# Kernel optimization log

Hardware: AMD Instinct MI355X
Metric: run time of the kernel (lower is better)

## Reference

```python
import jax, jax.numpy as jnp
import numpy as np

EMB = 1024
HEADS = 16


def setup_inputs() -> dict:
    key = jax.random.key(0)
    k1, k2, k3, k4, k5 = jax.random.split(key, 5)
    b, n = 2, 2048
    x = jax.random.normal(k1, (b, n, EMB), dtype=jnp.float32)
    Wqkv = jax.random.normal(k2, (EMB, 3 * EMB), dtype=jnp.float32) * (EMB ** -0.5)
    bqkv = jax.random.normal(k3, (3 * EMB,), dtype=jnp.float32) * 0.02
    Wproj = jax.random.normal(k4, (EMB, EMB), dtype=jnp.float32) * (EMB ** -0.5)
    bproj = jax.random.normal(k5, (EMB,), dtype=jnp.float32) * 0.02
    return {"x": x, "Wqkv": Wqkv, "bqkv": bqkv, "Wproj": Wproj, "bproj": bproj}


def reference(x, Wqkv, bqkv, Wproj, bproj):
    b, n, e = x.shape
    h = HEADS
    d = e // h
    qkv = x @ Wqkv + bqkv                      # [b, n, 3e]
    # rearrange 'b n (h d qkv) -> qkv b h n d' : qkv index is innermost
    qkv = qkv.reshape(b, n, h, d, 3)
    qkv = jnp.transpose(qkv, (4, 0, 2, 1, 3))  # [3, b, h, n, d]
    q, k, v = qkv[0], qkv[1], qkv[2]
    energy = jnp.einsum('bhqd,bhkd->bhqk', q, k)
    scaling = jnp.float32(e) ** 0.5            # NOTE: sqrt(emb_size), not head_dim
    att = jax.nn.softmax(energy / scaling, axis=-1)
    out = jnp.einsum('bhql,bhld->bhqd', att, v)
    out = jnp.transpose(out, (0, 2, 1, 3)).reshape(b, n, e)  # 'b h n d -> b n (h d)'
    return out @ Wproj + bproj
```

## Files before the change

kernel.cpp:

```cpp
#include <hip/hip_runtime.h>
#include <hip/hip_bf16.h>
#include <stdint.h>

typedef __bf16 bf16;
typedef __attribute__((ext_vector_type(8))) __bf16 bf16x8;
typedef __attribute__((ext_vector_type(4))) __bf16 bf16x4;
typedef __attribute__((ext_vector_type(4))) float f32x4;
typedef __attribute__((ext_vector_type(16))) float f32x16;

#define MFMA16(a, b, c) __builtin_amdgcn_mfma_f32_16x16x32_bf16((a), (b), (c), 0, 0, 0)
#define MFMA32(a, b, c) __builtin_amdgcn_mfma_f32_32x32x16_bf16((a), (b), (c), 0, 0, 0)

#define QSCALE 0.045084220027780106f

__device__ __forceinline__ void glds16(const void* g, void* l) {
  __builtin_amdgcn_global_load_lds(
      (const __attribute__((address_space(1))) void*)g,
      (__attribute__((address_space(3))) void*)l, 16, 0, 0);
}

__device__ __forceinline__ bf16x8 ldsfrag(const unsigned char* base, int row, int colb) {
  return *(const bf16x8*)(base + row * 128 + (colb ^ ((row & 7) << 4)));
}

__device__ __forceinline__ uint32_t pkbf16(float a, float b) {
  uint32_t r;
  asm("v_cvt_pk_bf16_f32 %0, %1, %2" : "=v"(r) : "v"(a), "v"(b));
  return r;
}

__device__ __forceinline__ float fexp2(float x) {
#if __has_builtin(__builtin_amdgcn_exp2f)
  return __builtin_amdgcn_exp2f(x);
#else
  float r;
  asm("v_exp_f32 %0, %1" : "=v"(r) : "v"(x));
  return r;
#endif
}

__device__ __forceinline__ f32x16 zero16() {
  f32x16 v;
#pragma unroll
  for (int i = 0; i < 16; ++i) v[i] = 0.f;
  return v;
}

__global__ __launch_bounds__(256) void k_prep_x(const float* __restrict__ x, bf16* __restrict__ xb) {
  int gid = blockIdx.x * 256 + threadIdx.x;
  const f32x4* xv = (const f32x4*)x;
  f32x4 a = xv[(size_t)gid * 2], b = xv[(size_t)gid * 2 + 1];
  bf16x8 o;
#pragma unroll
  for (int i = 0; i < 4; ++i) { o[i] = (bf16)a[i]; o[i + 4] = (bf16)b[i]; }
  *(bf16x8*)(xb + (size_t)gid * 8) = o;
}

template <int MODE>
__global__ __launch_bounds__(256) void k_prep_w(const float* __restrict__ W, bf16* __restrict__ WT) {
  __shared__ float tile[64][256];
  const int C = (MODE == 0) ? 3072 : 1024;
  const int c0 = blockIdx.x * 256, k0 = blockIdx.y * 64;
  const int lw = threadIdx.x & 63, w = threadIdx.x >> 6;
#pragma unroll
  for (int i = 0; i < 16; ++i) {
    int r = i * 4 + w;
    f32x4 v = *(const f32x4*)(W + (size_t)(k0 + r) * C + c0 + lw * 4);
    *(f32x4*)&tile[r][lw * 4] = v;
  }
  __syncthreads();
  const int c = c0 + threadIdx.x;
  int j;
  float sc = 1.0f;
  if (MODE == 0) {
    int h = c / 192, rem = c - h * 192, dd = rem / 3, wh = rem - dd * 3;
    j = wh * 1024 + h * 64 + dd;
    if (wh == 0) sc = QSCALE;
  } else {
    j = c;
  }
#pragma unroll
  for (int ch = 0; ch < 8; ++ch) {
    bf16x8 o;
#pragma unroll
    for (int i = 0; i < 8; ++i) o[i] = (bf16)(tile[ch * 8 + i][threadIdx.x] * sc);
    *(bf16x8*)(WT + (size_t)j * 1024 + k0 + ch * 8) = o;
  }
}

__global__ __launch_bounds__(256) void k_prep_bias(const float* __restrict__ bqkv, float* __restrict__ bp) {
  int gid = blockIdx.x * 256 + threadIdx.x;
  int wj = gid >> 10, rr = gid & 1023, hh = rr >> 6, d2 = rr & 63;
  float v = bqkv[hh * 192 + d2 * 3 + wj];
  bp[gid] = (wj == 0) ? v * QSCALE : v;
}

template <int EPI>
__global__ __launch_bounds__(256) void k_gemm(const bf16* __restrict__ A, const bf16* __restrict__ BT,
                                              const float* __restrict__ bias, bf16* __restrict__ qk,
                                              bf16* __restrict__ vt, float* __restrict__ outf) {
  __shared__ __align__(16) unsigned char sA[16384];
  __shared__ __align__(16) unsigned char sB[16384];
  const int tid = threadIdx.x;
  const int l = tid & 63, w = tid >> 6, g = l >> 4, l15 = l & 15;
  const int wr = w >> 1, wc = w & 1;
  const int bm = blockIdx.y, bn = blockIdx.x;
  const unsigned char* Ab = (const unsigned char*)A + (size_t)bm * 128 * 2048;
  const unsigned char* Bb = (const unsigned char*)BT + (size_t)bn * 128 * 2048;
  f32x4 acc[4][4];
#pragma unroll
  for (int mi = 0; mi < 4; ++mi)
#pragma unroll
    for (int ni = 0; ni < 4; ++ni) acc[mi][ni] = (f32x4){0.f, 0.f, 0.f, 0.f};

  for (int kt = 0; kt < 16; ++kt) {
    const int k0b = kt * 128;
#pragma unroll
    for (int p = 0; p < 4; ++p) {
      int co = (p * 256 + tid) * 16;
      int row = co >> 7, wb = co & 127;
      int sw = wb ^ ((row & 7) << 4);
      glds16(Ab + (size_t)row * 2048 + k0b + sw, sA + co);
      glds16(Bb + (size_t)row * 2048 + k0b + sw, sB + co);
    }
    __syncthreads();
#pragma unroll
    for (int ks = 0; ks < 2; ++ks) {
      bf16x8 af[4], bfr[4];
#pragma unroll
      for (int mi = 0; mi < 4; ++mi) af[mi] = ldsfrag(sA, wr * 64 + mi * 16 + l15, ks * 64 + g * 16);
#pragma unroll
      for (int ni = 0; ni < 4; ++ni) bfr[ni] = ldsfrag(sB, wc * 64 + ni * 16 + l15, ks * 64 + g * 16);
      __builtin_amdgcn_s_setprio(1);
#pragma unroll
      for (int mi = 0; mi < 4; ++mi)
#pragma unroll
        for (int ni = 0; ni < 4; ++ni) acc[mi][ni] = MFMA16(af[mi], bfr[ni], acc[mi][ni]);
      __builtin_amdgcn_s_setprio(0);
    }
    __syncthreads();
  }
#pragma unroll
  for (int ni = 0; ni < 4; ++ni) {
    int j = bn * 128 + wc * 64 + ni * 16 + l15;
    float bj = bias[j];
#pragma unroll
    for (int mi = 0; mi < 4; ++mi) {
      int m0 = bm * 128 + wr * 64 + mi * 16 + g * 4;
      float v[4];
#pragma unroll
      for (int rr = 0; rr < 4; ++rr) v[rr] = acc[mi][ni][rr] + bj;
      if (EPI == 0) {
        int which = j >> 10, r = j & 1023, h = r >> 6, dd = r & 63;
        int b = m0 >> 11, nn = m0 & 2047;
        if (which < 2) {
#pragma unroll
          for (int rr = 0; rr < 4; ++rr)
            qk[(size_t)which * 4194304 + (((size_t)b * 16 + h) * 2048 + nn + rr) * 64 + dd] = (bf16)v[rr];
        } else {
          bf16x4 pw = {(bf16)v[0], (bf16)v[1], (bf16)v[2], (bf16)v[3]};
          *(bf16x4*)(vt + (((size_t)b * 16 + h) * 64 + dd) * 2048 + nn) = pw;
        }
      } else {
#pragma unroll
        for (int rr = 0; rr < 4; ++rr) outf[(size_t)(m0 + rr) * 1024 + j] = v[rr];
      }
    }
  }
}

__global__ __launch_bounds__(256, 2) void k_attn(const bf16* __restrict__ Qg, const bf16* __restrict__ Kg,
                                                 const bf16* __restrict__ VTg, bf16* __restrict__ Og) {
  __shared__ __align__(16) unsigned char smem[66560];
  const int tid = threadIdx.x;
  const int l = tid & 63, w = tid >> 6;
  const int q = l & 31, hi = l >> 5;
  const int g = w >> 1, wl = w & 1;
  const int stid = tid & 127;

  const int bid = blockIdx.x;
  const int wg = (bid & 7) * 64 + (bid >> 3);
  const int bh = wg >> 4;
  const int q0w = (wg & 15) * 128 + wl * 64;

  bf16x8 qf[2][4];
#pragma unroll
  for (int qt = 0; qt < 2; ++qt)
#pragma unroll
    for (int ks = 0; ks < 4; ++ks)
      qf[qt][ks] = *(const bf16x8*)(Qg + ((size_t)bh * 2048 + q0w + qt * 32 + q) * 64 + ks * 16 + hi * 8);

  f32x16 oacc[2][2];
#pragma unroll
  for (int qt = 0; qt < 2; ++qt) { oacc[qt][0] = zero16(); oacc[qt][1] = zero16(); }
  float lrun4[2][4] = {{0.f, 0.f, 0.f, 0.f}, {0.f, 0.f, 0.f, 0.f}};
  bf16x8 pb[2][4];

  const unsigned char* Kb = (const unsigned char*)Kg + (size_t)bh * 262144 + (size_t)g * 131072;
  const unsigned char* Vb = (const unsigned char*)VTg + (size_t)bh * 262144 + (size_t)g * 2048;
  unsigned char* sKg = smem + g * 16384;
  unsigned char* sVg = smem + 32768 + g * 16384;

  int sco[4], ssw[4];
  size_t svoff[4];
#pragma unroll
  for (int i = 0; i < 4; ++i) {
    sco[i] = stid * 16 + i * 2048;
    int row = sco[i] >> 7;
    ssw[i] = (sco[i] & 127) ^ ((row & 7) << 4);
    svoff[i] = (size_t)row * 4096 + ssw[i];
  }

#define STAGE_K(kb_, buf_)                                                        \
  do {                                                                            \
    const unsigned char* Ksrc = Kb + (size_t)(kb_) * 8192;                        \
    _Pragma("unroll") for (int i = 0; i < 4; ++i)                                 \
      glds16(Ksrc + (sco[i] & ~127) + ssw[i], sKg + (buf_) * 8192 + sco[i]);      \
  } while (0)
#define STAGE_V(kb_, buf_)                                                        \
  do {                                                                            \
    _Pragma("unroll") for (int i = 0; i < 4; ++i)                                 \
      glds16(Vb + svoff[i] + (size_t)(kb_) * 128, sVg + (buf_) * 8192 + sco[i]);  \
  } while (0)

#define QK_EXP_PACK(kbase_)                                                       \
  do {                                                                            \
    _Pragma("unroll") for (int kt = 0; kt < 2; ++kt) {                            \
      bf16x8 kf[4];                                                               \
      _Pragma("unroll") for (int ks = 0; ks < 4; ++ks)                            \
        kf[ks] = ldsfrag((kbase_), kt * 32 + q, ks * 32 + hi * 16);               \
      _Pragma("unroll") for (int qt = 0; qt < 2; ++qt) {                          \
        f32x16 sacc = zero16();                                                   \
        __builtin_amdgcn_s_setprio(1);                                            \
        _Pragma("unroll") for (int ks = 0; ks < 4; ++ks)                          \
          sacc = MFMA32(kf[ks], qf[qt][ks], sacc);                                \
        __builtin_amdgcn_s_setprio(0);                                            \
        float pe[16];                                                             \
        _Pragma("unroll") for (int r = 0; r < 16; ++r) pe[r] = fexp2(sacc[r]);    \
        _Pragma("unroll") for (int m = 0; m < 4; ++m)                             \
          _Pragma("unroll") for (int j = 0; j < 4; ++j) lrun4[qt][j] += pe[4 * m + j]; \
        uint32_t c[4][2];                                                         \
        _Pragma("unroll") for (int m = 0; m < 4; ++m) {                           \
          c[m][0] = pkbf16(pe[4 * m], pe[4 * m + 1]);                             \
          c[m][1] = pkbf16(pe[4 * m + 2], pe[4 * m + 3]);                         \
        }                                                                         \
        _Pragma("unroll") for (int s = 0; s < 2; ++s) {                           \
          uint32_t x0 = c[2 * s][0], y0 = c[2 * s + 1][0];                        \
          uint32_t x1 = c[2 * s][1], y1 = c[2 * s + 1][1];                        \
          asm("v_permlane32_swap_b32 %0, %1" : "+v"(x0), "+v"(y0));               \
          asm("v_permlane32_swap_b32 %0, %1" : "+v"(x1), "+v"(y1));               \
          union { uint32_t u[4]; bf16x8 v; } bfr;                                 \
          bfr.u[0] = x0; bfr.u[1] = x1; bfr.u[2] = y0; bfr.u[3] = y1;             \
          pb[qt][kt * 2 + s] = bfr.v;                                             \
        }                                                                         \
      }                                                                           \
    }                                                                             \
  } while (0)

#define PV_TILE(vbase_)                                                           \
  do {                                                                            \
    __builtin_amdgcn_s_setprio(1);                                                \
    _Pragma("unroll") for (int ks = 0; ks < 4; ++ks)                              \
      _Pragma("unroll") for (int dt = 0; dt < 2; ++dt) {                          \
        bf16x8 vf = ldsfrag((vbase_), dt * 32 + q, ks * 32 + hi * 16);            \
        _Pragma("unroll") for (int qt = 0; qt < 2; ++qt)                          \
          oacc[qt][dt] = MFMA32(vf, pb[qt][ks], oacc[qt][dt]);                    \
      }                                                                           \
    __builtin_amdgcn_s_setprio(0);                                                \
  } while (0)

  STAGE_K(0, 0);
  STAGE_V(0, 0);
  __syncthreads();
  STAGE_K(1, 1);
  QK_EXP_PACK(sKg);
  __syncthreads();
  int cur = 0;

  for (int kb = 0; kb < 15; ++kb) {
    const int nxt = cur ^ 1;
    if (kb < 14) STAGE_K(kb + 2, cur);
    STAGE_V(kb + 1, nxt);
    PV_TILE(sVg + cur * 8192);
    QK_EXP_PACK(sKg + nxt * 8192);
    __syncthreads();
    cur = nxt;
  }
  PV_TILE(sVg + cur * 8192);

#undef STAGE_K
#undef STAGE_V
#undef QK_EXP_PACK
#undef PV_TILE

  float lrun[2];
#pragma unroll
  for (int qt = 0; qt < 2; ++qt)
    lrun[qt] = (lrun4[qt][0] + lrun4[qt][1]) + (lrun4[qt][2] + lrun4[qt][3]);

  float* mbuf = (float*)smem;
  float* lb = (float*)(smem + 65536);
  if (g == 1) {
#pragma unroll
    for (int qt = 0; qt < 2; ++qt) {
#pragma unroll
      for (int dt = 0; dt < 2; ++dt)
#pragma unroll
        for (int r = 0; r < 16; ++r)
          mbuf[((wl * 64 + qt * 32 + dt * 16 + r) << 6) + l] = oacc[qt][dt][r];
      lb[(wl * 2 + qt) * 64 + l] = lrun[qt];
    }
  }
  __syncthreads();
  if (g == 0) {
#pragma unroll
    for (int qt = 0; qt < 2; ++qt)
#pragma unroll
      for (int dt = 0; dt < 2; ++dt)
#pragma unroll
        for (int r = 0; r < 16; ++r)
          oacc[qt][dt][r] += mbuf[((wl * 64 + qt * 32 + dt * 16 + r) << 6) + l];
  }
  __syncthreads();
  if (g == 0) {
    const int b = bh >> 4, h = bh & 15;
    unsigned char* sO = smem + 32768 + wl * 4096;
#pragma unroll
    for (int qt = 0; qt < 2; ++qt) {
      float lr = lrun[qt] + lb[(wl * 2 + qt) * 64 + l];
      float ps = lr + __shfl_xor(lr, 32);
      float linv = 1.0f / ps;
#pragma unroll
      for (int dt = 0; dt < 2; ++dt)
#pragma unroll
        for (int m = 0; m < 4; ++m) {
          uint32_t b0 = pkbf16(oacc[qt][dt][4 * m] * linv, oacc[qt][dt][4 * m + 1] * linv);
          uint32_t b1 = pkbf16(oacc[qt][dt][4 * m + 2] * linv, oacc[qt][dt][4 * m + 3] * linv);
          int byteo = (dt * 64 + m * 16 + hi * 8) ^ ((q & 7) << 4);
          uint32_t* dst = (uint32_t*)(sO + q * 128 + byteo);
          dst[0] = b0; dst[1] = b1;
        }
      const int q0 = q0w + qt * 32;
#pragma unroll
      for (int rd = 0; rd < 4; ++rd) {
        int byteo = hi * 64 + rd * 16;
        bf16x8 v = *(const bf16x8*)(sO + q * 128 + (byteo ^ ((q & 7) << 4)));
        *(bf16x8*)(Og + ((size_t)b * 2048 + q0 + q) * 1024 + h * 64 + byteo / 2) = v;
      }
    }
  }
}

extern "C" void kernel_launch(void* const* d_in, const int* in_sizes, int n_in,
                              void* d_out, int out_size, void* d_ws, size_t ws_size,
                              hipStream_t stream) {
  const float* x = (const float*)d_in[0];
  const float* Wqkv = (const float*)d_in[1];
  const float* bqkv = (const float*)d_in[2];
  const float* Wproj = (const float*)d_in[3];
  const float* bproj = (const float*)d_in[4];
  float* out = (float*)d_out;
  char* ws = (char*)d_ws;

  bf16* XB = (bf16*)(ws + 0);
  bf16* WQT = (bf16*)(ws + 8388608);
  float* BQP = (float*)(ws + 14680064);
  bf16* WPT = (bf16*)(ws + 14696448);
  bf16* Q = (bf16*)(ws + 16793600);
  bf16* K = (bf16*)(ws + 25182208);
  bf16* VT = (bf16*)(ws + 33570816);
  bf16* AO = XB;
  (void)K;
  (void)ws_size;

  k_prep_x<<<2048, 256, 0, stream>>>(x, XB);
  k_prep_w<0><<<dim3(12, 16), 256, 0, stream>>>(Wqkv, WQT);
  k_prep_w<1><<<dim3(4, 16), 256, 0, stream>>>(Wproj, WPT);
  k_prep_bias<<<12, 256, 0, stream>>>(bqkv, BQP);
  k_gemm<0><<<dim3(24, 32), 256, 0, stream>>>(XB, WQT, BQP, Q, VT, nullptr);
  k_attn<<<512, 256, 0, stream>>>(Q, Q + 4194304, VT, AO);
  k_gemm<1><<<dim3(8, 32), 256, 0, stream>>>(AO, WPT, bproj, nullptr, nullptr, out);
}
```

Baseline: 125.3 us.

## Interleave PV MFMAs with QK/exp work using ping-pong probability registers

The main attention loop now interleaves the PV matrix multiplies for the previous key block with the QK scores and exponentials of the next block inside one fused iteration. Probabilities go into two alternating register sets (pbA/pbB), and the loop is unrolled by two so the buffer indices are compile-time constants. The aim is to hide exp/pack VALU latency behind MFMA work and give the scheduler more overlap. In exchange it needs more VGPRs for the second probability buffer, which could lower occupancy or cause spills.

```diff
diff --git a/kernel.cpp b/kernel.cpp
--- a/kernel.cpp
+++ b/kernel.cpp
@@ -194,7 +194,7 @@
 #pragma unroll
   for (int qt = 0; qt < 2; ++qt) { oacc[qt][0] = zero16(); oacc[qt][1] = zero16(); }
   float lrun4[2][4] = {{0.f, 0.f, 0.f, 0.f}, {0.f, 0.f, 0.f, 0.f}};
-  bf16x8 pb[2][4];
+  bf16x8 pbA[2][4], pbB[2][4];
 
   const unsigned char* Kb = (const unsigned char*)Kg + (size_t)bh * 262144 + (size_t)g * 131072;
   const unsigned char* Vb = (const unsigned char*)VTg + (size_t)bh * 262144 + (size_t)g * 2048;
@@ -223,7 +223,7 @@
       glds16(Vb + svoff[i] + (size_t)(kb_) * 128, sVg + (buf_) * 8192 + sco[i]);  \
   } while (0)
 
-#define QK_EXP_PACK(kbase_)                                                       \
+#define QK_EXP_PACK(kbase_, PBOUT)                                                \
   do {                                                                            \
     _Pragma("unroll") for (int kt = 0; kt < 2; ++kt) {                            \
       bf16x8 kf[4];                                                               \
@@ -251,47 +251,88 @@
           asm("v_permlane32_swap_b32 %0, %1" : "+v"(x1), "+v"(y1));               \
           union { uint32_t u[4]; bf16x8 v; } bfr;                                 \
           bfr.u[0] = x0; bfr.u[1] = x1; bfr.u[2] = y0; bfr.u[3] = y1;             \
-          pb[qt][kt * 2 + s] = bfr.v;                                             \
+          PBOUT[qt][kt * 2 + s] = bfr.v;                                          \
         }                                                                         \
       }                                                                           \
     }                                                                             \
   } while (0)
 
-#define PV_TILE(vbase_)                                                           \
+#define PV_TILE(vbase_, PB)                                                       \
   do {                                                                            \
     __builtin_amdgcn_s_setprio(1);                                                \
     _Pragma("unroll") for (int ks = 0; ks < 4; ++ks)                              \
       _Pragma("unroll") for (int dt = 0; dt < 2; ++dt) {                          \
         bf16x8 vf = ldsfrag((vbase_), dt * 32 + q, ks * 32 + hi * 16);            \
-        _Pragma("unroll") for (int qt = 0; qt < 2; ++qt)                          \
-          oacc[qt][dt] = MFMA32(vf, pb[qt][ks], oacc[qt][dt]);                    \
+        _Pragma("unroll") for (int qtp = 0; qtp < 2; ++qtp)                       \
+          oacc[qtp][dt] = MFMA32(vf, PB[qtp][ks], oacc[qtp][dt]);                 \
       }                                                                           \
     __builtin_amdgcn_s_setprio(0);                                                \
+  } while (0)
+
+#define ITER(kb_, CUR, PBIN, PBOUT)                                               \
+  do {                                                                            \
+    if ((kb_) < 14) STAGE_K((kb_) + 2, CUR);                                      \
+    STAGE_V((kb_) + 1, (CUR) ^ 1);                                                \
+    const unsigned char* kqb = sKg + ((CUR) ^ 1) * 8192;                          \
+    const unsigned char* vpb = sVg + (CUR) * 8192;                                \
+    _Pragma("unroll") for (int kt = 0; kt < 2; ++kt) {                            \
+      bf16x8 kf[4];                                                               \
+      _Pragma("unroll") for (int ks = 0; ks < 4; ++ks)                            \
+        kf[ks] = ldsfrag(kqb, kt * 32 + q, ks * 32 + hi * 16);                    \
+      _Pragma("unroll") for (int qt = 0; qt < 2; ++qt) {                          \
+        const int ksq = kt * 2 + qt;                                              \
+        f32x16 sacc = zero16();                                                   \
+        __builtin_amdgcn_s_setprio(1);                                            \
+        _Pragma("unroll") for (int ks = 0; ks < 4; ++ks)                          \
+          sacc = MFMA32(kf[ks], qf[qt][ks], sacc);                                \
+        _Pragma("unroll") for (int dt = 0; dt < 2; ++dt) {                        \
+          bf16x8 vf = ldsfrag(vpb, dt * 32 + q, ksq * 32 + hi * 16);              \
+          _Pragma("unroll") for (int qtp = 0; qtp < 2; ++qtp)                     \
+            oacc[qtp][dt] = MFMA32(vf, PBIN[qtp][ksq], oacc[qtp][dt]);            \
+        }                                                                         \
+        __builtin_amdgcn_s_setprio(0);                                            \
+        float pe[16];                                                             \
+        _Pragma("unroll") for (int r = 0; r < 16; ++r) pe[r] = fexp2(sacc[r]);    \
+        _Pragma("unroll") for (int m = 0; m < 4; ++m)                             \
+          _Pragma("unroll") for (int j = 0; j < 4; ++j) lrun4[qt][j] += pe[4 * m + j]; \
+        uint32_t c[4][2];                                                         \
+        _Pragma("unroll") for (int m = 0; m < 4; ++m) {                           \
+          c[m][0] = pkbf16(pe[4 * m], pe[4 * m + 1]);                             \
+          c[m][1] = pkbf16(pe[4 * m + 2], pe[4 * m + 3]);                         \
+        }                                                                         \
+        _Pragma("unroll") for (int s = 0; s < 2; ++s) {                           \
+          uint32_t x0 = c[2 * s][0], y0 = c[2 * s + 1][0];                        \
+          uint32_t x1 = c[2 * s][1], y1 = c[2 * s + 1][1];                        \
+          asm("v_permlane32_swap_b32 %0, %1" : "+v"(x0), "+v"(y0));               \
+          asm("v_permlane32_swap_b32 %0, %1" : "+v"(x1), "+v"(y1));               \
+          union { uint32_t u[4]; bf16x8 v; } bfr;                                 \
+          bfr.u[0] = x0; bfr.u[1] = x1; bfr.u[2] = y0; bfr.u[3] = y1;             \
+          PBOUT[qt][kt * 2 + s] = bfr.v;                                          \
+        }                                                                         \
+      }                                                                           \
+    }                                                                             \
+    __syncthreads();                                                              \
   } while (0)
 
   STAGE_K(0, 0);
   STAGE_V(0, 0);
   __syncthreads();
   STAGE_K(1, 1);
-  QK_EXP_PACK(sKg);
+  QK_EXP_PACK(sKg, pbA);
   __syncthreads();
-  int cur = 0;
-
-  for (int kb = 0; kb < 15; ++kb) {
-    const int nxt = cur ^ 1;
-    if (kb < 14) STAGE_K(kb + 2, cur);
-    STAGE_V(kb + 1, nxt);
-    PV_TILE(sVg + cur * 8192);
-    QK_EXP_PACK(sKg + nxt * 8192);
-    __syncthreads();
-    cur = nxt;
-  }
-  PV_TILE(sVg + cur * 8192);
+
+  for (int kb2 = 0; kb2 < 7; ++kb2) {
+    ITER(kb2 * 2, 0, pbA, pbB);
+    ITER(kb2 * 2 + 1, 1, pbB, pbA);
+  }
+  ITER(14, 0, pbA, pbB);
+  PV_TILE(sVg + 8192, pbB);
 
 #undef STAGE_K
 #undef STAGE_V
 #undef QK_EXP_PACK
 #undef PV_TILE
+#undef ITER
 
   float lrun[2];
 #pragma unroll
```

Result: no change. 127.7 us (+1.9%).
